# Kernel optimization log

Measured on AMD Instinct MI355X. Metric: run time of the kernel, lower is better.

Reference implementation:

```python
import jax, jax.numpy as jnp
import numpy as np

VOXEL_SIZE = np.array([0.2, 0.2, 4.0], dtype=np.float32)
PC_MIN = np.array([0.0, -40.0, -3.0], dtype=np.float32)
BN_EPS = 1e-3
N_POINTS = 1_500_000
N_VOXELS = 200_000
C_IN = 7   # (4 - 3) + 6 stats channels (cluster offset + voxel-center offset)
C_OUT = 64


def setup_inputs() -> dict:
    key = jax.random.key(0)
    ks = jax.random.split(key, 8)
    features = jax.random.normal(ks[0], (N_POINTS, 4), dtype=jnp.float32)
    point2voxel = jax.random.randint(ks[1], (N_POINTS,), 0, N_VOXELS).astype(jnp.int32)
    voxel_coors = jnp.stack([
        jax.random.randint(ks[2], (N_VOXELS,), 0, 2),    # batch idx
        jnp.zeros((N_VOXELS,), jnp.int32),               # z (pillars -> 0)
        jax.random.randint(ks[3], (N_VOXELS,), 0, 400),  # y bin
        jax.random.randint(ks[4], (N_VOXELS,), 0, 352),  # x bin
    ], axis=1).astype(jnp.int32)
    W = jax.random.normal(ks[5], (C_IN, C_OUT), dtype=jnp.float32) * 0.1
    bn_gamma = jnp.ones((C_OUT,), jnp.float32)
    bn_beta = jnp.zeros((C_OUT,), jnp.float32)
    bn_mean = jax.random.normal(ks[6], (C_OUT,), dtype=jnp.float32) * 0.01
    bn_var = jax.random.uniform(ks[7], (C_OUT,), minval=0.5, maxval=1.5, dtype=jnp.float32)
    return dict(features=features, W=W, bn_gamma=bn_gamma, bn_beta=bn_beta,
                bn_mean=bn_mean, bn_var=bn_var, point2voxel=point2voxel,
                voxel_coors=voxel_coors)


def reference(features, W, bn_gamma, bn_beta, bn_mean, bn_var, point2voxel, voxel_coors):
    M = voxel_coors.shape[0]
    xyz = features[:, :3]

    # --- stats: cluster-center offset (per-voxel mean of xyz, mapped back) ---
    cnt = jax.ops.segment_sum(jnp.ones((xyz.shape[0],), xyz.dtype), point2voxel,
                              num_segments=M)
    vmean = jax.ops.segment_sum(xyz, point2voxel, num_segments=M)
    vmean = vmean / jnp.maximum(cnt, 1.0)[:, None]
    cluster_off = xyz - vmean[point2voxel]

    # --- stats: voxel-center offset ---
    vs = jnp.asarray(VOXEL_SIZE)
    mn = jnp.asarray(PC_MIN)
    # coors layout is (batch, z, y, x) -> take (x, y, z)
    centers = (voxel_coors[:, jnp.array([3, 2, 1])].astype(jnp.float32) + 0.5) * vs + mn
    center_off = xyz - centers[point2voxel]

    feats = jnp.concatenate([cluster_off, center_off, features[:, 3:]], axis=-1)  # [N,7]

    # --- PFN layer: Linear(bias=False) + BN1d (eval stats) + ReLU ---
    h = feats @ W
    h = (h - bn_mean) * jax.lax.rsqrt(bn_var + BN_EPS) * bn_gamma + bn_beta
    h = jax.nn.relu(h)

    # --- scatter max-reduce to voxels ---
    vfeats = jax.ops.segment_max(h, point2voxel, num_segments=M)
    vfeats = jnp.where(jnp.isfinite(vfeats), vfeats, 0.0)  # guard rare empty voxels
    return vfeats, voxel_coors
```

## Files before the change

### kernel.cpp

```cpp
#include <hip/hip_runtime.h>


#define BBITS 6
#define BVOX  (1 << BBITS)
#define PCAP  768
#define NR    (PCAP / 256)
#define NBLK  256
#define BMAX  3200
#define SCH   4096

__global__ __launch_bounds__(256) void hist_k(const int* __restrict__ p2v,
                                              int* __restrict__ mat,
                                              int N, int NB, int chunk) {
    __shared__ int h[BMAX];
    int b = blockIdx.x, tid = threadIdx.x;
    for (int k = tid; k < NB; k += 256) h[k] = 0;
    __syncthreads();
    int s = b * chunk, e = min(N, s + chunk);
    for (int i = s + tid; i < e; i += 256)
        atomicAdd(&h[p2v[i] >> BBITS], 1);
    __syncthreads();
    for (int k = tid; k < NB; k += 256) mat[k * NBLK + b] = h[k];
}

__global__ void scanA_k(int* __restrict__ a, int* __restrict__ bsum, int S) {
    __shared__ int s[256];
    int tid = threadIdx.x;
    int base = blockIdx.x * SCH + tid * 16;
    int c[16];
    int tsum = 0;
#pragma unroll
    for (int j = 0; j < 16; ++j) {
        c[j] = (base + j < S) ? a[base + j] : 0;
        tsum += c[j];
    }
    s[tid] = tsum;
    __syncthreads();
    for (int off = 1; off < 256; off <<= 1) {
        int v = (tid >= off) ? s[tid - off] : 0;
        __syncthreads();
        s[tid] += v;
        __syncthreads();
    }
    int run = s[tid] - tsum;
#pragma unroll
    for (int j = 0; j < 16; ++j) {
        if (base + j < S) a[base + j] = run;
        run += c[j];
    }
    if (tid == 255) bsum[blockIdx.x] = s[255];
}

__global__ void scanB_k(int* __restrict__ bsum, int nb) {
    __shared__ int s[256];
    int tid = threadIdx.x;
    int v = (tid < nb) ? bsum[tid] : 0;
    s[tid] = v;
    __syncthreads();
    for (int off = 1; off < 256; off <<= 1) {
        int t = (tid >= off) ? s[tid - off] : 0;
        __syncthreads();
        s[tid] += t;
        __syncthreads();
    }
    if (tid < nb) bsum[tid] = s[tid] - v;
}

__global__ void scanC_k(int* __restrict__ a, const int* __restrict__ bsum, int S) {
    int i = blockIdx.x * blockDim.x + threadIdx.x;
    if (i < S) a[i] += bsum[i / SCH];
}

__global__ __launch_bounds__(256) void scatter_kidx_k(const int* __restrict__ p2v,
                                                      const int* __restrict__ mat,
                                                      int* __restrict__ keyidx,
                                                      int N, int NB, int chunk) {
    __shared__ int cur[BMAX];
    int b = blockIdx.x, tid = threadIdx.x;
    for (int k = tid; k < NB; k += 256) cur[k] = mat[k * NBLK + b];
    __syncthreads();
    int s = b * chunk, e = min(N, s + chunk);
    for (int i = s + tid; i < e; i += 256) {
        int v = p2v[i];
        int k = v >> BBITS;
        int pos = atomicAdd(&cur[k], 1);
        keyidx[pos] = (i << BBITS) | (v & (BVOX - 1));
    }
}

__global__ __launch_bounds__(256, 8) void gather_bucket_k(
    const float4* __restrict__ feats, const int* __restrict__ keyidx,
    const int* __restrict__ mat, const float* __restrict__ W,
    const float* __restrict__ gamma, const float* __restrict__ beta,
    const float* __restrict__ mean, const float* __restrict__ var,
    const int* __restrict__ coors,
    float* __restrict__ out_v, float* __restrict__ out_c,
    int M, int NB, int N) {
    __shared__ float4 s_pay[PCAP];
    __shared__ int    s_cnt[BVOX];
    __shared__ int    s_off[BVOX];
    __shared__ int    s_cur[BVOX];
    __shared__ float4 s_cen[BVOX];

    int bk = blockIdx.x, tid = threadIdx.x;
    int lane = tid & 63, w = tid >> 6;

    float w0 = W[0 * 64 + lane], w1 = W[1 * 64 + lane], w2 = W[2 * 64 + lane];
    float w3 = W[3 * 64 + lane], w4 = W[4 * 64 + lane], w5 = W[5 * 64 + lane];
    float w6 = W[6 * 64 + lane];
    float sc = gamma[lane] * rsqrtf(var[lane] + 1e-3f);
    float bi = beta[lane] - mean[lane] * sc;
    float sgn = (sc >= 0.0f) ? 1.0f : -1.0f;
    float u0 = sgn * (w0 + w3), u1 = sgn * (w1 + w4);
    float u2 = sgn * (w2 + w5), u3 = sgn * w6;

    int s = mat[bk * NBLK];
    int e = (bk + 1 < NB) ? mat[(bk + 1) * NBLK] : N;
    int L = min(e - s, PCAP);

    int pk[NR];
    float4 fv[NR];
#pragma unroll
    for (int r = 0; r < NR; ++r) {
        int j = tid + r * 256;
        pk[r] = (j < L) ? keyidx[s + j] : -1;
    }
#pragma unroll
    for (int r = 0; r < NR; ++r)
        if (pk[r] >= 0) fv[r] = feats[pk[r] >> BBITS];

    if (tid < BVOX) s_cnt[tid] = 0;
    __syncthreads();
#pragma unroll
    for (int r = 0; r < NR; ++r)
        if (pk[r] >= 0) atomicAdd(&s_cnt[pk[r] & (BVOX - 1)], 1);

    int vbase = bk << BBITS;
    if (tid < BVOX) {
        int vg = vbase + tid;
        if (vg < M) {
            int4 cc = ((const int4*)coors)[vg];
            ((float4*)out_c)[vg] = make_float4((float)cc.x, (float)cc.y,
                                               (float)cc.z, (float)cc.w);
            s_cen[tid] = make_float4((cc.w + 0.5f) * 0.2f,
                                     (cc.z + 0.5f) * 0.2f - 40.0f,
                                     (cc.y + 0.5f) * 4.0f - 3.0f, 0.0f);
        }
    }
    __syncthreads();

    if (w == 0) {
        int c = s_cnt[lane];
        int x = c;
        for (int off = 1; off < 64; off <<= 1) {
            int t = __shfl_up(x, off);
            if (lane >= off) x += t;
        }
        int ex = x - c;
        s_off[lane] = ex;
        s_cur[lane] = ex;
    }
    __syncthreads();

#pragma unroll
    for (int r = 0; r < NR; ++r)
        if (pk[r] >= 0) {
            int vox = pk[r] & (BVOX - 1);
            int pos = atomicAdd(&s_cur[vox], 1);
            s_pay[pos] = fv[r];
        }
    __syncthreads();

    int lv0 = w << 4;
    int cnts[16];
#pragma unroll
    for (int q = 0; q < 16; ++q) cnts[q] = s_cnt[lv0 + q];
    int st = s_off[lv0];

    for (int q = 0; q < 16; ++q) {
        int lv = lv0 + q;
        int v = vbase + lv;
        int npts = cnts[q];
        float4 cen = s_cen[lv];
        float sx = 0.f, sy = 0.f, sz = 0.f;
        float amax = -3.402823466e+38f;
        int i = 0;
        for (; i + 3 < npts; i += 4) {
            float4 f0 = s_pay[st + i + 0];
            float4 f1 = s_pay[st + i + 1];
            float4 f2 = s_pay[st + i + 2];
            float4 f3 = s_pay[st + i + 3];
            sx += f0.x + f1.x + f2.x + f3.x;
            sy += f0.y + f1.y + f2.y + f3.y;
            sz += f0.z + f1.z + f2.z + f3.z;
            float a0 = f0.x * u0 + f0.y * u1 + f0.z * u2 + f0.w * u3;
            float a1 = f1.x * u0 + f1.y * u1 + f1.z * u2 + f1.w * u3;
            float a2 = f2.x * u0 + f2.y * u1 + f2.z * u2 + f2.w * u3;
            float a3 = f3.x * u0 + f3.y * u1 + f3.z * u2 + f3.w * u3;
            amax = fmaxf(fmaxf(fmaxf(amax, a0), fmaxf(a1, a2)), a3);
        }
        for (; i < npts; ++i) {
            float4 f = s_pay[st + i];
            sx += f.x; sy += f.y; sz += f.z;
            float a = f.x * u0 + f.y * u1 + f.z * u2 + f.w * u3;
            amax = fmaxf(amax, a);
        }
        float res = 0.0f;
        if (npts > 0) {
            float inv = 1.0f / (float)npts;
            float mx = sx * inv, my = sy * inv, mz = sz * inv;
            float K = mx * w0 + my * w1 + mz * w2 +
                      cen.x * w3 + cen.y * w4 + cen.z * w5;
            float aext = sgn * amax;
            res = fmaxf((aext - K) * sc + bi, 0.0f);
        }
        if (v < M) out_v[(size_t)v * 64 + lane] = res;
        st += npts;
    }
}

extern "C" void kernel_launch(void* const* d_in, const int* in_sizes, int n_in,
                              void* d_out, int out_size, void* d_ws, size_t ws_size,
                              hipStream_t stream) {
    const float* features = (const float*)d_in[0];
    const float* W        = (const float*)d_in[1];
    const float* gamma    = (const float*)d_in[2];
    const float* beta     = (const float*)d_in[3];
    const float* mean     = (const float*)d_in[4];
    const float* var      = (const float*)d_in[5];
    const int*   p2v      = (const int*)d_in[6];
    const int*   coors    = (const int*)d_in[7];
    int N = in_sizes[0] / 4;
    int M = in_sizes[7] / 4;

    int NB = (M + BVOX - 1) >> BBITS;
    int S = NB * NBLK;
    int chunk = (N + NBLK - 1) / NBLK;

    int* mat    = (int*)d_ws;
    int* bsum   = mat + S;
    int* keyidx = bsum + 256;

    float* out_v = (float*)d_out;
    float* out_c = out_v + (size_t)M * 64;

    hist_k<<<NBLK, 256, 0, stream>>>(p2v, mat, N, NB, chunk);
    int nbA = (S + SCH - 1) / SCH;
    scanA_k<<<nbA, 256, 0, stream>>>(mat, bsum, S);
    scanB_k<<<1, 256, 0, stream>>>(bsum, nbA);
    scanC_k<<<(S + 255) / 256, 256, 0, stream>>>(mat, bsum, S);
    scatter_kidx_k<<<NBLK, 256, 0, stream>>>(p2v, mat, keyidx, N, NB, chunk);
    gather_bucket_k<<<NB, 256, 0, stream>>>(
        (const float4*)features, keyidx, mat, W, gamma, beta, mean, var,
        coors, out_v, out_c, M, NB, N);
}
```

Baseline: 135.5 us.

## Double voxel bucket size, transpose histogram matrix, fold scan fixup into consumers

Buckets now hold 128 voxels instead of 64, with the payload cap raised to 1280 points, which halves the number of buckets and the size of the histogram matrix. The histogram is stored block-major so hist_k writes contiguously, and scanA reads it through transposed indices. The separate scanC pass is removed: scatter_kidx_k and gather_bucket_k now add the block-sum offset themselves. In exchange, scan accesses become strided, the in-block voxel prefix scan uses shared memory with block-wide barriers, and the occupancy hint drops from 8 to 4 blocks per SM.

```diff
diff --git a/kernel.cpp b/kernel.cpp
--- a/kernel.cpp
+++ b/kernel.cpp
@@ -1,12 +1,12 @@
 #include <hip/hip_runtime.h>
 
 
-#define BBITS 6
+#define BBITS 7
 #define BVOX  (1 << BBITS)
-#define PCAP  768
+#define PCAP  1280
 #define NR    (PCAP / 256)
 #define NBLK  256
-#define BMAX  3200
+#define BMAX  1600
 #define SCH   4096
 
 __global__ __launch_bounds__(256) void hist_k(const int* __restrict__ p2v,
@@ -20,18 +20,27 @@
     for (int i = s + tid; i < e; i += 256)
         atomicAdd(&h[p2v[i] >> BBITS], 1);
     __syncthreads();
-    for (int k = tid; k < NB; k += 256) mat[k * NBLK + b] = h[k];
-}
-
-__global__ void scanA_k(int* __restrict__ a, int* __restrict__ bsum, int S) {
+    for (int k = tid; k < NB; k += 256) mat[b * NB + k] = h[k];
+}
+
+__global__ void scanA_k(int* __restrict__ mat, int* __restrict__ bsum,
+                        int NB, int S) {
     __shared__ int s[256];
     int tid = threadIdx.x;
     int base = blockIdx.x * SCH + tid * 16;
-    int c[16];
+    int idx[16], c[16];
     int tsum = 0;
 #pragma unroll
     for (int j = 0; j < 16; ++j) {
-        c[j] = (base + j < S) ? a[base + j] : 0;
+        int p = base + j;
+        if (p < S) {
+            int k = p >> 8, b = p & 255;
+            idx[j] = b * NB + k;
+            c[j] = mat[idx[j]];
+        } else {
+            idx[j] = -1;
+            c[j] = 0;
+        }
         tsum += c[j];
     }
     s[tid] = tsum;
@@ -45,7 +54,7 @@
     int run = s[tid] - tsum;
 #pragma unroll
     for (int j = 0; j < 16; ++j) {
-        if (base + j < S) a[base + j] = run;
+        if (idx[j] >= 0) mat[idx[j]] = run;
         run += c[j];
     }
     if (tid == 255) bsum[blockIdx.x] = s[255];
@@ -66,18 +75,15 @@
     if (tid < nb) bsum[tid] = s[tid] - v;
 }
 
-__global__ void scanC_k(int* __restrict__ a, const int* __restrict__ bsum, int S) {
-    int i = blockIdx.x * blockDim.x + threadIdx.x;
-    if (i < S) a[i] += bsum[i / SCH];
-}
-
 __global__ __launch_bounds__(256) void scatter_kidx_k(const int* __restrict__ p2v,
                                                       const int* __restrict__ mat,
+                                                      const int* __restrict__ bsum,
                                                       int* __restrict__ keyidx,
                                                       int N, int NB, int chunk) {
     __shared__ int cur[BMAX];
     int b = blockIdx.x, tid = threadIdx.x;
-    for (int k = tid; k < NB; k += 256) cur[k] = mat[k * NBLK + b];
+    for (int k = tid; k < NB; k += 256)
+        cur[k] = mat[b * NB + k] + bsum[((k << 8) | b) >> 12];
     __syncthreads();
     int s = b * chunk, e = min(N, s + chunk);
     for (int i = s + tid; i < e; i += 256) {
@@ -88,9 +94,10 @@
     }
 }
 
-__global__ __launch_bounds__(256, 8) void gather_bucket_k(
+__global__ __launch_bounds__(256, 4) void gather_bucket_k(
     const float4* __restrict__ feats, const int* __restrict__ keyidx,
-    const int* __restrict__ mat, const float* __restrict__ W,
+    const int* __restrict__ mat, const int* __restrict__ bsum,
+    const float* __restrict__ W,
     const float* __restrict__ gamma, const float* __restrict__ beta,
     const float* __restrict__ mean, const float* __restrict__ var,
     const int* __restrict__ coors,
@@ -114,8 +121,8 @@
     float u0 = sgn * (w0 + w3), u1 = sgn * (w1 + w4);
     float u2 = sgn * (w2 + w5), u3 = sgn * w6;
 
-    int s = mat[bk * NBLK];
-    int e = (bk + 1 < NB) ? mat[(bk + 1) * NBLK] : N;
+    int s = mat[bk] + bsum[(bk << 8) >> 12];
+    int e = (bk + 1 < NB) ? (mat[bk + 1] + bsum[((bk + 1) << 8) >> 12]) : N;
     int L = min(e - s, PCAP);
 
     int pk[NR];
@@ -149,16 +156,18 @@
     }
     __syncthreads();
 
-    if (w == 0) {
-        int c = s_cnt[lane];
-        int x = c;
-        for (int off = 1; off < 64; off <<= 1) {
-            int t = __shfl_up(x, off);
-            if (lane >= off) x += t;
-        }
-        int ex = x - c;
-        s_off[lane] = ex;
-        s_cur[lane] = ex;
+    if (tid < BVOX) s_off[tid] = s_cnt[tid];
+    __syncthreads();
+    for (int off = 1; off < BVOX; off <<= 1) {
+        int t = (tid < BVOX && tid >= off) ? s_off[tid - off] : 0;
+        __syncthreads();
+        if (tid < BVOX) s_off[tid] += t;
+        __syncthreads();
+    }
+    if (tid < BVOX) {
+        int ex = s_off[tid] - s_cnt[tid];
+        s_off[tid] = ex;
+        s_cur[tid] = ex;
     }
     __syncthreads();
 
@@ -171,16 +180,13 @@
         }
     __syncthreads();
 
-    int lv0 = w << 4;
-    int cnts[16];
-#pragma unroll
-    for (int q = 0; q < 16; ++q) cnts[q] = s_cnt[lv0 + q];
+    int lv0 = w << 5;
     int st = s_off[lv0];
 
-    for (int q = 0; q < 16; ++q) {
+    for (int q = 0; q < 32; ++q) {
         int lv = lv0 + q;
         int v = vbase + lv;
-        int npts = cnts[q];
+        int npts = s_cnt[lv];
         float4 cen = s_cen[lv];
         float sx = 0.f, sy = 0.f, sz = 0.f;
         float amax = -3.402823466e+38f;
@@ -246,11 +252,10 @@
 
     hist_k<<<NBLK, 256, 0, stream>>>(p2v, mat, N, NB, chunk);
     int nbA = (S + SCH - 1) / SCH;
-    scanA_k<<<nbA, 256, 0, stream>>>(mat, bsum, S);
+    scanA_k<<<nbA, 256, 0, stream>>>(mat, bsum, NB, S);
     scanB_k<<<1, 256, 0, stream>>>(bsum, nbA);
-    scanC_k<<<(S + 255) / 256, 256, 0, stream>>>(mat, bsum, S);
-    scatter_kidx_k<<<NBLK, 256, 0, stream>>>(p2v, mat, keyidx, N, NB, chunk);
+    scatter_kidx_k<<<NBLK, 256, 0, stream>>>(p2v, mat, bsum, keyidx, N, NB, chunk);
     gather_bucket_k<<<NB, 256, 0, stream>>>(
-        (const float4*)features, keyidx, mat, W, gamma, beta, mean, var,
+        (const float4*)features, keyidx, mat, bsum, W, gamma, beta, mean, var,
         coors, out_v, out_c, M, NB, N);
 }
```

Result: faster. 125.6 us (-7.3%).
